# Kernel optimization log

Hardware: AMD Instinct MI355X
Metric: run time of the kernel (lower is better)

Reference implementation:

```python
import jax, jax.numpy as jnp
import numpy as np

D_NODE, D_EDGE, D_MODEL, TOPK, N_HEADS = 64, 16, 256, 5, 4
HEAD_DIM = D_MODEL // N_HEADS


def setup_inputs() -> dict:
    key = jax.random.key(0)
    ks = jax.random.split(key, 24)
    B, N = 256, 512
    E = N - 1
    def lin(k, fi, fo):
        k1, k2 = jax.random.split(k)
        s = 1.0 / np.sqrt(fi)
        return (jax.random.uniform(k1, (fi, fo), jnp.float32, -s, s),
                jax.random.uniform(k2, (fo,), jnp.float32, -s, s))
    Wn, bn = lin(ks[0], 8, D_NODE)
    We, be = lin(ks[1], 3, D_EDGE)
    Wq, bq = lin(ks[2], D_NODE, D_MODEL)
    Wkv, bkv = lin(ks[3], 2 * D_NODE + D_EDGE, 2 * D_MODEL)
    # MultiheadAttention in/out projections (fixed shared weights)
    Wiq, biq = lin(ks[4], D_MODEL, D_MODEL)
    Wik, bik = lin(ks[5], D_MODEL, D_MODEL)
    Wiv, biv = lin(ks[6], D_MODEL, D_MODEL)
    Wo, bo = lin(ks[7], D_MODEL, D_MODEL)
    Wf1, bf1 = lin(ks[8], D_NODE + D_MODEL, D_MODEL)
    Wf2, bf2 = lin(ks[9], D_MODEL, D_MODEL)
    Ws1, bs1 = lin(ks[10], D_NODE + D_EDGE + D_MODEL, D_MODEL)
    Ws2, bs2 = lin(ks[11], D_MODEL, 1 + 6 * D_MODEL)
    node_raw = jax.random.normal(ks[12], (B, N, 8), jnp.float32)
    edge_raw = jax.random.normal(ks[13], (B, E, 3), jnp.float32)
    return dict(node_raw=node_raw, edge_raw=edge_raw, ego_id=0,
                Wn=Wn, bn=bn, We=We, be=be, Wq=Wq, bq=bq, Wkv=Wkv, bkv=bkv,
                Wiq=Wiq, biq=biq, Wik=Wik, bik=bik, Wiv=Wiv, biv=biv,
                Wo=Wo, bo=bo, Wf1=Wf1, bf1=bf1, Wf2=Wf2, bf2=bf2,
                Ws1=Ws1, bs1=bs1, Ws2=Ws2, bs2=bs2)


def reference(node_raw, edge_raw, ego_id,
              Wn, bn, We, be, Wq, bq, Wkv, bkv,
              Wiq, biq, Wik, bik, Wiv, biv, Wo, bo,
              Wf1, bf1, Wf2, bf2, Ws1, bs1, Ws2, bs2):
    B, N, _ = node_raw.shape
    E = N - 1
    ego_id = int(ego_id)
    idx = np.arange(N)
    neighbor_idx = jnp.asarray(idx[idx != ego_id])  # (E,)

    node_feat = node_raw @ Wn + bn                   # (B, N, d_node)
    edge_feat = edge_raw @ We + be                   # (B, E, d_edge)
    ego_feat = node_feat[:, ego_id]                  # (B, d_node)
    neighbor_feat = node_feat[:, neighbor_idx]       # (B, E, d_node)

    ego_bcast = jnp.broadcast_to(ego_feat[:, None, :], (B, E, D_NODE))
    edge_input = jnp.concatenate([ego_bcast, edge_feat, neighbor_feat], -1)

    Q = ego_feat @ Wq + bq                           # (B, d_model)
    kv = edge_input @ Wkv + bkv                      # (B, E, 2*d_model)
    K, V = kv[..., :D_MODEL], kv[..., D_MODEL:]

    # MultiheadAttention: single query per batch, E keys/values
    q = (Q @ Wiq + biq).reshape(B, N_HEADS, HEAD_DIM)
    k = (K @ Wik + bik).reshape(B, E, N_HEADS, HEAD_DIM)
    v = (V @ Wiv + biv).reshape(B, E, N_HEADS, HEAD_DIM)
    scores = jnp.einsum('bhd,behd->bhe', q, k) / np.sqrt(HEAD_DIM)
    attn = jax.nn.softmax(scores, axis=-1)           # (B, H, E)
    ctx = jnp.einsum('bhe,behd->bhd', attn, v).reshape(B, D_MODEL)
    c_ego = ctx @ Wo + bo                            # (B, d_model)

    h = jnp.concatenate([ego_feat, c_ego], -1)
    h_ego_prime = jax.nn.relu(h @ Wf1 + bf1) @ Wf2 + bf2  # (B, d_model)

    c_bcast = jnp.broadcast_to(c_ego[:, None, :], (B, E, D_MODEL))
    edge_input2 = jnp.concatenate([neighbor_feat, edge_feat, c_bcast], -1)
    score_out = jax.nn.relu(edge_input2 @ Ws1 + bs1) @ Ws2 + bs2  # (B,E,1+6*dm)
    score = score_out[..., 0]                        # (B, E)
    h_enc = score_out[..., 1:].reshape(B, E, 6, D_MODEL)

    topk_val, topk_idx = jax.lax.top_k(score, TOPK)  # (B, topk)
    selected = jnp.take_along_axis(h_enc, topk_idx[:, :, None, None], axis=1)
    alpha = jax.nn.softmax(topk_val, axis=-1)[:, :, None, None]  # (B,topk,1,1)
    selected = selected * alpha
    return h_ego_prime, selected, topk_idx, alpha
```

## Files before the change

### kernel.cpp

```cpp
#include <hip/hip_runtime.h>
#include <hip/hip_bf16.h>
#include <math.h>

constexpr int B = 256, NN = 512, EE = 511;

constexpr size_t F_NF    = 0;
constexpr size_t F_EF    = F_NF   + (size_t)B*NN*64;
constexpr size_t F_WCK   = F_EF   + (size_t)B*EE*16;
constexpr size_t F_BCK   = F_WCK  + 144*256;
constexpr size_t F_WCV   = F_BCK  + 256;
constexpr size_t F_BCV   = F_WCV  + 144*256;
constexpr size_t F_WQ2   = F_BCV  + 256;
constexpr size_t F_BQ2   = F_WQ2  + 64*256;
constexpr size_t F_Q     = F_BQ2  + 256;
constexpr size_t F_AW    = F_Q    + (size_t)B*256;
constexpr size_t F_C0    = F_AW   + (size_t)B*4*80;
constexpr size_t F_SC    = F_C0   + (size_t)B*4;
constexpr size_t F_US    = F_SC   + (size_t)B*4*EE;
constexpr size_t F_CEGO  = F_US   + (size_t)B*4*80;
constexpr size_t F_CVEC  = F_CEGO + (size_t)B*256;
constexpr size_t F_SC2   = F_CVEC + (size_t)B*256;
constexpr size_t F_ALPHA = F_SC2  + (size_t)B*EE;
constexpr size_t F_TKI   = F_ALPHA+ (size_t)B*5;
constexpr size_t F_HS    = F_SC;

constexpr size_t O_HEGO  = 0;
constexpr size_t O_SEL   = 65536;
constexpr size_t O_TKI   = 2031616;
constexpr size_t O_ALPHA = 2032896;

__global__ void k_fuse(const float* Wkv, const float* bkv, const float* Wik, const float* bik,
                       const float* Wiv, const float* biv, const float* Wq,  const float* bq,
                       const float* Wiq, const float* biq, float* ws){
  int t = blockIdx.x*256 + threadIdx.x;
  if (t < 36864){
    int r = t >> 8, c = t & 255;
    float a = 0.f;
    for (int m=0;m<256;m++) a += Wkv[(size_t)r*512+m] * Wik[(size_t)m*256+c];
    ws[F_WCK + t] = a;
  } else if (t < 37120){
    int c = t - 36864;
    float a = bik[c];
    for (int m=0;m<256;m++) a += bkv[m] * Wik[(size_t)m*256+c];
    ws[F_BCK + c] = a;
  } else if (t < 73984){
    int i = t - 37120; int r = i >> 8, c = i & 255;
    float a = 0.f;
    for (int m=0;m<256;m++) a += Wkv[(size_t)r*512+256+m] * Wiv[(size_t)m*256+c];
    ws[F_WCV + i] = a;
  } else if (t < 74240){
    int c = t - 73984;
    float a = biv[c];
    for (int m=0;m<256;m++) a += bkv[256+m] * Wiv[(size_t)m*256+c];
    ws[F_BCV + c] = a;
  } else if (t < 90624){
    int i = t - 74240; int r = i >> 8, c = i & 255;
    float a = 0.f;
    for (int m=0;m<256;m++) a += Wq[(size_t)r*256+m] * Wiq[(size_t)m*256+c];
    ws[F_WQ2 + i] = a;
  } else if (t < 90880){
    int c = t - 90624;
    float a = biq[c];
    for (int m=0;m<256;m++) a += bq[m] * Wiq[(size_t)m*256+c];
    ws[F_BQ2 + c] = a;
  }
}

__global__ void k_nf(const float* node_raw, const float* Wn, const float* bn, float* ws){
  size_t t = (size_t)blockIdx.x*256 + threadIdx.x;
  int j = (int)(t & 63); size_t row = t >> 6;
  float a = bn[j];
  #pragma unroll
  for (int i=0;i<8;i++) a += node_raw[row*8+i] * Wn[(size_t)i*64+j];
  ws[F_NF + t] = a;
}

__global__ void k_ef(const float* edge_raw, const float* We, const float* be, float* ws){
  size_t t = (size_t)blockIdx.x*256 + threadIdx.x;
  int j = (int)(t & 15); size_t row = t >> 4;
  float a = be[j];
  #pragma unroll
  for (int i=0;i<3;i++) a += edge_raw[row*3+i] * We[(size_t)i*16+j];
  ws[F_EF + t] = a;
}

__global__ void k_head(const int* ego_p, float* ws){
  int b = blockIdx.x >> 2, h = blockIdx.x & 3;
  int tid = threadIdx.x;
  __shared__ float qh[64];
  __shared__ float red[256];
  int ego = *ego_p;
  const float* egf = ws + F_NF + ((size_t)b*NN+ego)*64;
  if (tid < 64){
    int c = h*64 + tid;
    float a = ws[F_BQ2 + c];
    for (int i=0;i<64;i++) a += egf[i]*ws[F_WQ2 + (size_t)i*256 + c];
    qh[tid] = a;
  }
  __syncthreads();
  const float* Wck = ws + F_WCK;
  float p = 0.f;
  size_t awbase = F_AW + ((size_t)(b*4+h))*80;
  if (tid < 64){
    const float* wr = Wck + (size_t)(80+tid)*256 + h*64;
    float a=0.f; for(int d=0;d<64;d++) a += wr[d]*qh[d];
    ws[awbase + tid] = a;
  } else if (tid < 80){
    int i = tid-64;
    const float* wr = Wck + (size_t)(64+i)*256 + h*64;
    float a=0.f; for(int d=0;d<64;d++) a += wr[d]*qh[d];
    ws[awbase + 64 + i] = a;
  } else if (tid < 144){
    int j = tid-80;
    const float* wr = Wck + (size_t)j*256 + h*64;
    float a=0.f; for(int d=0;d<64;d++) a += wr[d]*qh[d];
    p = egf[j] * a;
  } else if (tid < 208){
    int d = tid-144;
    p = ws[F_BCK + h*64 + d] * qh[d];
  }
  red[tid]=p; __syncthreads();
  for (int s=128;s>0;s>>=1){ if(tid<s) red[tid]+=red[tid+s]; __syncthreads(); }
  if (tid==0) ws[F_C0 + b*4 + h] = red[0];
}

__global__ void k_scores(const int* ego_p, float* ws){
  int tile = blockIdx.x, b = blockIdx.y, tid = threadIdx.x;
  __shared__ float awz[4][80];
  __shared__ float c0s[4];
  for (int l=tid; l<320; l+=256) awz[l/80][l%80] = ws[F_AW + (size_t)b*320 + l];
  if (tid<4) c0s[tid] = ws[F_C0 + b*4 + tid];
  __syncthreads();
  int e = tile*256 + tid;
  if (e >= EE) return;
  int ego = *ego_p;
  int node = e < ego ? e : e+1;
  const float4* nr = (const float4*)(ws + F_NF + ((size_t)b*NN+node)*64);
  const float4* er = (const float4*)(ws + F_EF + ((size_t)b*EE+e)*16);
  float s[4] = {c0s[0],c0s[1],c0s[2],c0s[3]};
  #pragma unroll
  for (int i=0;i<16;i++){
    float4 x = nr[i];
    #pragma unroll
    for (int h=0;h<4;h++)
      s[h] += x.x*awz[h][i*4] + x.y*awz[h][i*4+1] + x.z*awz[h][i*4+2] + x.w*awz[h][i*4+3];
  }
  #pragma unroll
  for (int i=0;i<4;i++){
    float4 x = er[i];
    #pragma unroll
    for (int h=0;h<4;h++)
      s[h] += x.x*awz[h][64+i*4] + x.y*awz[h][64+i*4+1] + x.z*awz[h][64+i*4+2] + x.w*awz[h][64+i*4+3];
  }
  #pragma unroll
  for (int h=0;h<4;h++) ws[F_SC + ((size_t)(b*4+h))*EE + e] = s[h]*0.125f;
}

__global__ void k_attn(const int* ego_p, float* ws){
  int bh = blockIdx.x; int b = bh>>2; int tid = threadIdx.x;
  __shared__ float sc[512];
  __shared__ float red[256];
  const float* s = ws + F_SC + (size_t)bh*EE;
  float v0 = tid<EE ? s[tid] : -INFINITY;
  float v1 = (tid+256)<EE ? s[tid+256] : -INFINITY;
  red[tid] = fmaxf(v0,v1); __syncthreads();
  for (int st=128;st>0;st>>=1){ if(tid<st) red[tid]=fmaxf(red[tid],red[tid+st]); __syncthreads(); }
  float m = red[0]; __syncthreads();
  float e0 = tid<EE ? expf(v0-m) : 0.f;
  float e1 = (tid+256)<EE ? expf(v1-m) : 0.f;
  red[tid] = e0+e1; __syncthreads();
  for (int st=128;st>0;st>>=1){ if(tid<st) red[tid]+=red[tid+st]; __syncthreads(); }
  float inv = 1.f/red[0];
  sc[tid] = e0*inv;
  sc[tid+256] = e1*inv;
  __syncthreads();
  int ego = *ego_p;
  if (tid < 64){
    const float* base = ws + F_NF + (size_t)b*NN*64 + tid;
    float a = 0.f;
    for (int e=0;e<EE;e++){
      int node = e<ego?e:e+1;
      a += sc[e]*base[(size_t)node*64];
    }
    ws[F_US + (size_t)bh*80 + tid] = a;
  } else if (tid < 80){
    int d = tid-64;
    const float* base = ws + F_EF + (size_t)b*EE*16 + d;
    float a = 0.f;
    for (int e=0;e<EE;e++) a += sc[e]*base[(size_t)e*16];
    ws[F_US + (size_t)bh*80 + tid] = a;
  }
}

__global__ void k_bfinal(const int* ego_p,
                         const float* Wo, const float* bo,
                         const float* Wf1, const float* bf1p,
                         const float* Wf2, const float* bf2p,
                         const float* Ws1, const float* bs1,
                         float* ws, float* out){
  int b = blockIdx.x, t = threadIdx.x;
  __shared__ float ego_s[64], us_s[4][80], ctx_s[256], cego_s[256], hf_s[256];
  int ego = *ego_p;
  if (t < 64) ego_s[t] = ws[F_NF + ((size_t)b*NN+ego)*64 + t];
  for (int l=t; l<320; l+=256) us_s[l/80][l%80] = ws[F_US + (size_t)b*320 + l];
  __syncthreads();
  {
    int h = t >> 6;
    const float* Wcv = ws + F_WCV;
    float a = ws[F_BCV + t];
    for (int i=0;i<64;i++) a += ego_s[i]*Wcv[(size_t)i*256+t];
    for (int i=0;i<16;i++) a += us_s[h][64+i]*Wcv[(size_t)(64+i)*256+t];
    for (int i=0;i<64;i++) a += us_s[h][i]*Wcv[(size_t)(80+i)*256+t];
    ctx_s[t]=a;
  }
  __syncthreads();
  {
    float a = bo[t];
    for (int i=0;i<256;i++) a += ctx_s[i]*Wo[(size_t)i*256+t];
    cego_s[t]=a; ws[F_CEGO + (size_t)b*256+t]=a;
  }
  __syncthreads();
  {
    float a = bf1p[t];
    for (int i=0;i<64;i++)  a += ego_s[i]*Wf1[(size_t)i*256+t];
    for (int i=0;i<256;i++) a += cego_s[i]*Wf1[(size_t)(64+i)*256+t];
    hf_s[t]=fmaxf(a,0.f);
  }
  __syncthreads();
  {
    float a = bf2p[t];
    for (int i=0;i<256;i++) a += hf_s[i]*Wf2[(size_t)i*256+t];
    out[O_HEGO + (size_t)b*256+t] = a;
  }
  {
    float a = bs1[t];
    for (int i=0;i<256;i++) a += cego_s[i]*Ws1[(size_t)(80+i)*256+t];
    ws[F_CVEC + (size_t)b*256+t]=a;
  }
}

__global__ __launch_bounds__(512) void k_bigscore(const int* ego_p, const float* Ws1,
                                                  const float* Ws2, const float* bs2, float* ws){
  int tile = blockIdx.x, b = blockIdx.y;
  int tid = threadIdx.x;
  __shared__ float Fe[64][80];
  __shared__ float Bs[16][256];
  __shared__ float cv_s[256], w2_s[256];
  int ego = *ego_p;
  if (tid < 256){
    cv_s[tid] = ws[F_CVEC + (size_t)b*256 + tid];
    w2_s[tid] = Ws2[(size_t)tid*1537];
  }
  for (int l=tid; l<80*64; l+=512){
    int e = l/80, k = l - e*80;
    int eg = tile*64 + e;
    float v = 0.f;
    if (eg < EE){
      int node = eg<ego?eg:eg+1;
      v = (k<64) ? ws[F_NF + ((size_t)b*NN+node)*64 + k]
                 : ws[F_EF + ((size_t)b*EE+eg)*16 + (k-64)];
    }
    Fe[e][k] = v;
  }
  int tc = tid & 31, te = tid >> 5;
  float acc[4][8];
  #pragma unroll
  for (int i=0;i<4;i++)
    #pragma unroll
    for (int j=0;j<8;j++) acc[i][j]=0.f;

  for (int c=0;c<5;c++){
    __syncthreads();
    {
      float4* dst = (float4*)&Bs[0][0];
      const float4* s4 = (const float4*)(Ws1 + (size_t)(c*16)*256);
      dst[tid]       = s4[tid];
      dst[tid + 512] = s4[tid + 512];
    }
    __syncthreads();
    #pragma unroll
    for (int kk=0; kk<16; kk+=4){
      float A[4][4];
      #pragma unroll
      for (int i=0;i<4;i++){
        float4 t4 = *(const float4*)&Fe[te*4+i][c*16+kk];
        A[i][0]=t4.x; A[i][1]=t4.y; A[i][2]=t4.z; A[i][3]=t4.w;
      }
      #pragma unroll
      for (int q=0;q<4;q++){
        float4 b0 = *(const float4*)&Bs[kk+q][tc*4];
        float4 b1 = *(const float4*)&Bs[kk+q][128 + tc*4];
        float bw[8] = {b0.x,b0.y,b0.z,b0.w,b1.x,b1.y,b1.z,b1.w};
        #pragma unroll
        for (int i=0;i<4;i++)
          #pragma unroll
          for (int j=0;j<8;j++) acc[i][j] = fmaf(A[i][q], bw[j], acc[i][j]);
      }
    }
  }
  float bs20 = bs2[0];
  #pragma unroll
  for (int i=0;i<4;i++){
    float p = 0.f;
    #pragma unroll
    for (int j=0;j<4;j++){
      int col = tc*4 + j;
      float hcol = acc[i][j] + cv_s[col];
      p += fmaxf(hcol,0.f)*w2_s[col];
    }
    #pragma unroll
    for (int j=0;j<4;j++){
      int col = 128 + tc*4 + j;
      float hcol = acc[i][4+j] + cv_s[col];
      p += fmaxf(hcol,0.f)*w2_s[col];
    }
    #pragma unroll
    for (int m=16;m>0;m>>=1) p += __shfl_xor(p, m, 64);
    if (tc==0){
      int eg = tile*64 + te*4 + i;
      if (eg < EE) ws[F_SC2 + (size_t)b*EE + eg] = p + bs20;
    }
  }
}

__global__ void k_topk(float* ws, float* out){
  int b = blockIdx.x, tid = threadIdx.x;
  __shared__ float sv[256]; __shared__ int si[256];
  __shared__ float tv[8];   __shared__ int tix[8];
  const float* s = ws + F_SC2 + (size_t)b*EE;
  float v0 = tid<EE ? s[tid] : -INFINITY;       int i0 = tid;
  float v1 = (tid+256)<EE ? s[tid+256] : -INFINITY; int i1 = tid+256;
  for (int t=0;t<5;t++){
    float bvv; int bii;
    if (v0 > v1 || (v0==v1 && i0<i1)){ bvv=v0; bii=i0; } else { bvv=v1; bii=i1; }
    sv[tid]=bvv; si[tid]=bii; __syncthreads();
    for (int st=128; st>0; st>>=1){
      if (tid<st){
        float ov=sv[tid+st]; int oi=si[tid+st];
        if (ov > sv[tid] || (ov==sv[tid] && oi<si[tid])){ sv[tid]=ov; si[tid]=oi; }
      }
      __syncthreads();
    }
    if (tid==0){ tv[t]=sv[0]; tix[t]=si[0]; }
    __syncthreads();
    int w = tix[t];
    if (i0==w) v0=-INFINITY;
    if (i1==w) v1=-INFINITY;
    __syncthreads();
  }
  if (tid==0){
    float m = tv[0];
    float ex[5]; float sum=0.f;
    for (int t=0;t<5;t++){ ex[t]=expf(tv[t]-m); sum+=ex[t]; }
    for (int t=0;t<5;t++){
      float al = ex[t]/sum;
      ws[F_ALPHA + (size_t)b*5+t] = al;
      ((int*)(ws + F_TKI))[b*5+t] = tix[t];
      out[O_TKI   + (size_t)b*5+t] = (float)tix[t];
      out[O_ALPHA + (size_t)b*5+t] = al;
    }
  }
}

__global__ void k_hid(const int* ego_p, const float* Ws1, float* ws){
  int bt = blockIdx.x;
  int b = bt/5;
  int tid = threadIdx.x;
  __shared__ float fr[80];
  int e = ((const int*)(ws+F_TKI))[bt];
  int ego = *ego_p;
  int node = e<ego ? e : e+1;
  if (tid < 64)      fr[tid] = ws[F_NF + ((size_t)b*NN+node)*64 + tid];
  else if (tid < 80) fr[tid] = ws[F_EF + ((size_t)b*EE+e)*16 + (tid-64)];
  __syncthreads();
  float a = ws[F_CVEC + (size_t)b*256 + tid];
  for (int d=0;d<80;d++) a += fr[d]*Ws1[(size_t)d*256+tid];
  ws[F_HS + (size_t)bt*256 + tid] = fmaxf(a,0.f);
}

__global__ __launch_bounds__(256) void k_enc(const float* Ws2, const float* bs2,
                                             float* ws, float* out){
  int r = blockIdx.x, g = blockIdx.y, tid = threadIdx.x;
  int n = r*256 + tid;
  __shared__ float hs[10][256];
  __shared__ float al[10];
  int b0 = g*2;
  for (int l=tid; l<10*256; l+=256)
    hs[l>>8][l&255] = ws[F_HS + ((size_t)b0*5)*256 + l];
  if (tid<10) al[tid] = ws[F_ALPHA + (size_t)b0*5 + tid];
  __syncthreads();
  float acc[10];
  #pragma unroll
  for (int i=0;i<10;i++) acc[i]=0.f;
  const float* w2p = Ws2 + 1 + n;
  for (int j=0;j<256;j+=4){
    float w0 = w2p[(size_t)(j+0)*1537];
    float w1 = w2p[(size_t)(j+1)*1537];
    float w2 = w2p[(size_t)(j+2)*1537];
    float w3 = w2p[(size_t)(j+3)*1537];
    #pragma unroll
    for (int i=0;i<10;i++){
      float4 h = *(const float4*)&hs[i][j];
      acc[i] = fmaf(h.x,w0, fmaf(h.y,w1, fmaf(h.z,w2, fmaf(h.w,w3, acc[i]))));
    }
  }
  float bb = bs2[1+n];
  #pragma unroll
  for (int i=0;i<10;i++)
    out[O_SEL + ((size_t)(b0*5+i))*1536 + n] = (acc[i]+bb)*al[i];
}

extern "C" void kernel_launch(void* const* d_in, const int* in_sizes, int n_in,
                              void* d_out, int out_size, void* d_ws, size_t ws_size,
                              hipStream_t stream){
  const float* node_raw=(const float*)d_in[0];
  const float* edge_raw=(const float*)d_in[1];
  const int*  ego_p   =(const int*)d_in[2];
  const float* Wn =(const float*)d_in[3];  const float* bn =(const float*)d_in[4];
  const float* We =(const float*)d_in[5];  const float* be =(const float*)d_in[6];
  const float* Wq =(const float*)d_in[7];  const float* bq =(const float*)d_in[8];
  const float* Wkv=(const float*)d_in[9];  const float* bkv=(const float*)d_in[10];
  const float* Wiq=(const float*)d_in[11]; const float* biq=(const float*)d_in[12];
  const float* Wik=(const float*)d_in[13]; const float* bik=(const float*)d_in[14];
  const float* Wiv=(const float*)d_in[15]; const float* biv=(const float*)d_in[16];
  const float* Wo =(const float*)d_in[17]; const float* bo =(const float*)d_in[18];
  const float* Wf1=(const float*)d_in[19]; const float* bf1p=(const float*)d_in[20];
  const float* Wf2=(const float*)d_in[21]; const float* bf2p=(const float*)d_in[22];
  const float* Ws1=(const float*)d_in[23]; const float* bs1=(const float*)d_in[24];
  const float* Ws2=(const float*)d_in[25]; const float* bs2=(const float*)d_in[26];
  float* ws=(float*)d_ws;
  float* out=(float*)d_out;

  k_fuse<<<355,256,0,stream>>>(Wkv,bkv,Wik,bik,Wiv,biv,Wq,bq,Wiq,biq,ws);
  k_nf<<<(B*NN*64)/256,256,0,stream>>>(node_raw,Wn,bn,ws);
  k_ef<<<(B*EE*16)/256,256,0,stream>>>(edge_raw,We,be,ws);
  k_head<<<B*4,256,0,stream>>>(ego_p,ws);
  k_scores<<<dim3(2,B),256,0,stream>>>(ego_p,ws);
  k_attn<<<B*4,256,0,stream>>>(ego_p,ws);
  k_bfinal<<<B,256,0,stream>>>(ego_p,Wo,bo,Wf1,bf1p,Wf2,bf2p,Ws1,bs1,ws,out);
  k_bigscore<<<dim3(8,B),512,0,stream>>>(ego_p,Ws1,Ws2,bs2,ws);
  k_topk<<<B,256,0,stream>>>(ws,out);
  k_hid<<<B*5,256,0,stream>>>(ego_p,Ws1,ws);
  k_enc<<<dim3(6,128),256,0,stream>>>(Ws2,bs2,ws,out);
}
```

Baseline: 245.7 us.

## Merge feature kernels, split attention reduction across warps, double-buffer Ws1 tiles

Three separate changes. The node and edge feature projection kernels become one launch. The attention context reduction in k_attn now spreads the edge loop over all 256 threads in four groups and sums the partials in shared memory, where before only 80 threads did serial 511-step loops. k_bigscore register-prefetches the next Ws1 chunk into a double-buffered shared tile, which removes one barrier per chunk in exchange for more shared memory and registers.

After: 321.7 us. 30.9% more time.

```diff
diff --git a/kernel.cpp b/kernel.cpp
--- a/kernel.cpp
+++ b/kernel.cpp
@@ -66,22 +66,26 @@
   }
 }
 
-__global__ void k_nf(const float* node_raw, const float* Wn, const float* bn, float* ws){
-  size_t t = (size_t)blockIdx.x*256 + threadIdx.x;
-  int j = (int)(t & 63); size_t row = t >> 6;
-  float a = bn[j];
-  #pragma unroll
-  for (int i=0;i<8;i++) a += node_raw[row*8+i] * Wn[(size_t)i*64+j];
-  ws[F_NF + t] = a;
-}
-
-__global__ void k_ef(const float* edge_raw, const float* We, const float* be, float* ws){
-  size_t t = (size_t)blockIdx.x*256 + threadIdx.x;
-  int j = (int)(t & 15); size_t row = t >> 4;
-  float a = be[j];
-  #pragma unroll
-  for (int i=0;i<3;i++) a += edge_raw[row*3+i] * We[(size_t)i*16+j];
-  ws[F_EF + t] = a;
+constexpr int NFB = (B*NN*64)/256;
+constexpr int EFB = (B*EE*16)/256;
+__global__ void k_feat(const float* node_raw, const float* Wn, const float* bn,
+                       const float* edge_raw, const float* We, const float* be, float* ws){
+  int blk = blockIdx.x;
+  if (blk < NFB){
+    size_t t = (size_t)blk*256 + threadIdx.x;
+    int j = (int)(t & 63); size_t row = t >> 6;
+    float a = bn[j];
+    #pragma unroll
+    for (int i=0;i<8;i++) a += node_raw[row*8+i] * Wn[(size_t)i*64+j];
+    ws[F_NF + t] = a;
+  } else {
+    size_t t = (size_t)(blk-NFB)*256 + threadIdx.x;
+    int j = (int)(t & 15); size_t row = t >> 4;
+    float a = be[j];
+    #pragma unroll
+    for (int i=0;i<3;i++) a += edge_raw[row*3+i] * We[(size_t)i*16+j];
+    ws[F_EF + t] = a;
+  }
 }
 
 __global__ void k_head(const int* ego_p, float* ws){
@@ -160,6 +164,7 @@
   int bh = blockIdx.x; int b = bh>>2; int tid = threadIdx.x;
   __shared__ float sc[512];
   __shared__ float red[256];
+  __shared__ float part[4][80];
   const float* s = ws + F_SC + (size_t)bh*EE;
   float v0 = tid<EE ? s[tid] : -INFINITY;
   float v1 = (tid+256)<EE ? s[tid+256] : -INFINITY;
@@ -175,21 +180,26 @@
   sc[tid+256] = e1*inv;
   __syncthreads();
   int ego = *ego_p;
-  if (tid < 64){
-    const float* base = ws + F_NF + (size_t)b*NN*64 + tid;
+  {
+    int grp = tid >> 6, d = tid & 63;
+    const float* base = ws + F_NF + (size_t)b*NN*64 + d;
     float a = 0.f;
-    for (int e=0;e<EE;e++){
+    for (int e=grp; e<EE; e+=4){
       int node = e<ego?e:e+1;
       a += sc[e]*base[(size_t)node*64];
     }
-    ws[F_US + (size_t)bh*80 + tid] = a;
-  } else if (tid < 80){
-    int d = tid-64;
-    const float* base = ws + F_EF + (size_t)b*EE*16 + d;
+    part[grp][d] = a;
+  }
+  if (tid < 64){
+    int g2 = tid >> 4, d2 = tid & 15;
+    const float* base = ws + F_EF + (size_t)b*EE*16 + d2;
     float a = 0.f;
-    for (int e=0;e<EE;e++) a += sc[e]*base[(size_t)e*16];
-    ws[F_US + (size_t)bh*80 + tid] = a;
-  }
+    for (int e=g2; e<EE; e+=4) a += sc[e]*base[(size_t)e*16];
+    part[g2][64+d2] = a;
+  }
+  __syncthreads();
+  if (tid < 80)
+    ws[F_US + (size_t)bh*80 + tid] = part[0][tid]+part[1][tid]+part[2][tid]+part[3][tid];
 }
 
 __global__ void k_bfinal(const int* ego_p,
@@ -244,7 +254,7 @@
   int tile = blockIdx.x, b = blockIdx.y;
   int tid = threadIdx.x;
   __shared__ float Fe[64][80];
-  __shared__ float Bs[16][256];
+  __shared__ float Bs[2][16][256];
   __shared__ float cv_s[256], w2_s[256];
   int ego = *ego_p;
   if (tid < 256){
@@ -262,6 +272,11 @@
     }
     Fe[e][k] = v;
   }
+  const float4* W4 = (const float4*)Ws1;
+  float4 r0 = W4[tid], r1 = W4[tid+512];
+  { float4* dst = (float4*)&Bs[0][0][0]; dst[tid]=r0; dst[tid+512]=r1; }
+  r0 = W4[1024+tid]; r1 = W4[1024+tid+512];
+
   int tc = tid & 31, te = tid >> 5;
   float acc[4][8];
   #pragma unroll
@@ -271,13 +286,12 @@
 
   for (int c=0;c<5;c++){
     __syncthreads();
-    {
-      float4* dst = (float4*)&Bs[0][0];
-      const float4* s4 = (const float4*)(Ws1 + (size_t)(c*16)*256);
-      dst[tid]       = s4[tid];
-      dst[tid + 512] = s4[tid + 512];
-    }
-    __syncthreads();
+    if (c+1 < 5){
+      float4* dst = (float4*)&Bs[(c+1)&1][0][0];
+      dst[tid]=r0; dst[tid+512]=r1;
+      if (c+2 < 5){ r0 = W4[(size_t)(c+2)*1024+tid]; r1 = W4[(size_t)(c+2)*1024+tid+512]; }
+    }
+    const float (*Bc)[256] = Bs[c&1];
     #pragma unroll
     for (int kk=0; kk<16; kk+=4){
       float A[4][4];
@@ -288,8 +302,8 @@
       }
       #pragma unroll
       for (int q=0;q<4;q++){
-        float4 b0 = *(const float4*)&Bs[kk+q][tc*4];
-        float4 b1 = *(const float4*)&Bs[kk+q][128 + tc*4];
+        float4 b0 = *(const float4*)&Bc[kk+q][tc*4];
+        float4 b1 = *(const float4*)&Bc[kk+q][128 + tc*4];
         float bw[8] = {b0.x,b0.y,b0.z,b0.w,b1.x,b1.y,b1.z,b1.w};
         #pragma unroll
         for (int i=0;i<4;i++)
@@ -432,8 +446,7 @@
   float* out=(float*)d_out;
 
   k_fuse<<<355,256,0,stream>>>(Wkv,bkv,Wik,bik,Wiv,biv,Wq,bq,Wiq,biq,ws);
-  k_nf<<<(B*NN*64)/256,256,0,stream>>>(node_raw,Wn,bn,ws);
-  k_ef<<<(B*EE*16)/256,256,0,stream>>>(edge_raw,We,be,ws);
+  k_feat<<<NFB+EFB,256,0,stream>>>(node_raw,Wn,bn,edge_raw,We,be,ws);
   k_head<<<B*4,256,0,stream>>>(ego_p,ws);
   k_scores<<<dim3(2,B),256,0,stream>>>(ego_p,ws);
   k_attn<<<B*4,256,0,stream>>>(ego_p,ws);
```
